# Kernel optimization log

Measured on AMD Instinct MI355X. Metric: run time of the kernel, lower is better.

The kernel has to match this reference:

```python
import jax, jax.numpy as jnp
import numpy as np

FP8_MAX = 448.0  # max finite value of float8_e4m3fn


def _fp8_quant(v, scale):
    # emulate saturating scaled cast to float8_e4m3fn, then dequant-free fp8 storage (upcast to f32 for the gemm)
    q = jnp.clip(v / scale, -FP8_MAX, FP8_MAX)
    return q.astype(jnp.float8_e4m3fn).astype(jnp.float32)


def setup_inputs() -> dict:
    key = jax.random.key(0)
    k0, k1, k2, k3 = jax.random.split(key, 4)
    T, H, I, E = 1024, 1024, 2816, 8
    x = jax.random.normal(k0, (T, H), jnp.float32)
    router_logits = jax.random.normal(k1, (T, E), jnp.float32)
    w13_weight = jax.random.normal(k2, (E, 2 * I, H), jnp.float32) * 0.02
    w2_weight = jax.random.normal(k3, (E, H, I), jnp.float32) * 0.02
    return {
        "x": x,
        "router_logits": router_logits,
        "w13_weight": w13_weight,
        "w2_weight": w2_weight,
        "w13_input_scale": jnp.ones((E,), jnp.float32),
        "w2_input_scale": jnp.ones((E,), jnp.float32),
        "top_k": 2,
    }


def reference(x, router_logits, w13_weight, w2_weight, w13_input_scale, w2_input_scale, top_k):
    T, H = x.shape
    E, two_I, _ = w13_weight.shape
    I = two_I // 2

    # --- routing: softmax -> top_k -> renormalize (select_experts) ---
    probs = jax.nn.softmax(router_logits, axis=-1)
    topk_w, topk_ids = jax.lax.top_k(probs, top_k)            # [T,K]
    topk_w = topk_w / jnp.sum(topk_w, axis=-1, keepdims=True)
    # dense combine matrix [T,E]: sparsity of the grouped gemm dispatch
    combine = jnp.zeros((T, E), x.dtype).at[jnp.arange(T)[:, None], topk_ids].add(topk_w)

    # --- per-expert fp8 weight quantization (ops.scaled_fp8_quant per expert) ---
    w13_scale = jnp.max(jnp.abs(w13_weight), axis=(1, 2)) / FP8_MAX  # [E]
    w2_scale = jnp.max(jnp.abs(w2_weight), axis=(1, 2)) / FP8_MAX
    w13_q = _fp8_quant(w13_weight, w13_scale[:, None, None])         # [E,2I,H]
    w2_q = _fp8_quant(w2_weight, w2_scale[:, None, None])            # [E,H,I]

    # --- grouped gemm 1: per-expert activation quant + fp8 gemm + dequant scale ---
    x_q = _fp8_quant(x[None], w13_input_scale[:, None, None])        # [E,T,H]
    h = jnp.einsum('eth,eih->eti', x_q, w13_q) * (w13_input_scale * w13_scale)[:, None, None]

    # --- silu_and_mul: gate = first intermediate_size rows, up = second ---
    act = jax.nn.silu(h[..., :I]) * h[..., I:]                       # [E,T,I]

    # --- grouped gemm 2 ---
    act_q = _fp8_quant(act, w2_input_scale[:, None, None])
    o = jnp.einsum('eti,ehi->eth', act_q, w2_q) * (w2_input_scale * w2_scale)[:, None, None]

    # --- post_reorder: weighted combine of selected experts ---
    return jnp.einsum('te,eth->th', combine, o)                      # [T,H]
```

## Files before the change

### kernel.cpp

```cpp
#include <hip/hip_runtime.h>
#include <cstdint>
#include <cstddef>

#define T_TOK 1024
#define H_DIM 1024
#define I_DIM 2816
#define E_NUM 8
#define PAIRS 2048
#define KSPLIT 4
#define NT1 (I_DIM / 16)
#define AMX2_X 32

typedef __attribute__((ext_vector_type(4))) float f32x4;
typedef __attribute__((ext_vector_type(4))) unsigned int u32x4;
typedef long i64;

__device__ __forceinline__ unsigned char fp8e4m3_sw(float v) {
  v = fminf(448.f, fmaxf(-448.f, v));
  unsigned b = __float_as_uint(v);
  unsigned s = (b >> 24) & 0x80u;
  float a = fabsf(v);
  if (a < 0.015625f) {
    int m = (int)rintf(a * 512.f);
    return (unsigned char)(s | (unsigned)m);
  }
  unsigned ab = b & 0x7fffffffu;
  unsigned rnd = 0x7FFFFu + ((ab >> 20) & 1u);
  ab += rnd;
  int e = (int)(ab >> 23) - 127;
  unsigned m = (ab >> 20) & 7u;
  if (e > 8 || (e == 8 && m > 6)) { e = 8; m = 6; }
  return (unsigned char)(s | (unsigned)((e + 7) << 3) | m);
}

__device__ __forceinline__ unsigned q4(float a, float b, float c, float d) {
#if __has_builtin(__builtin_amdgcn_cvt_pk_fp8_f32)
  unsigned w = (unsigned)__builtin_amdgcn_cvt_pk_fp8_f32(a, b, 0, false);
  return (unsigned)__builtin_amdgcn_cvt_pk_fp8_f32(c, d, (int)w, true);
#else
  return (unsigned)fp8e4m3_sw(a) | ((unsigned)fp8e4m3_sw(b) << 8) |
         ((unsigned)fp8e4m3_sw(c) << 16) | ((unsigned)fp8e4m3_sw(d) << 24);
#endif
}

__device__ __forceinline__ unsigned char q1(float a) {
#if __has_builtin(__builtin_amdgcn_cvt_pk_fp8_f32)
  return (unsigned char)((unsigned)__builtin_amdgcn_cvt_pk_fp8_f32(a, a, 0, false) & 0xFFu);
#else
  return fp8e4m3_sw(a);
#endif
}

__device__ __forceinline__ unsigned q4v(float4 f, float inv) {
  return q4(f.x * inv, f.y * inv, f.z * inv, f.w * inv);
}

__device__ __forceinline__ float wave_max(float m) {
#pragma unroll
  for (int off = 32; off > 0; off >>= 1) m = fmaxf(m, __shfl_xor(m, off));
  return m;
}

__global__ __launch_bounds__(256) void pre_k(const float* __restrict__ w13,
                                             const float* __restrict__ logits,
                                             float* __restrict__ part13,
                                             int* __restrict__ cnt_g,
                                             int* __restrict__ offs_g,
                                             int* __restrict__ pair_tok,
                                             float* __restrict__ pair_w,
                                             int* __restrict__ pairidx) {
  const int tid = threadIdx.x;
  if (blockIdx.x < 1024) {
    const int e = blockIdx.x >> 7, sub = blockIdx.x & 127;
    const float4* src = (const float4*)w13 + (size_t)e * (2 * I_DIM * H_DIM / 4);
    int idx = sub * 256 + tid;
    const int stride = 128 * 256;
    float m = 0.f;
#pragma unroll
    for (int j = 0; j < 44; j += 4) {
      float4 v0 = src[idx + (size_t)(j + 0) * stride];
      float4 v1 = src[idx + (size_t)(j + 1) * stride];
      float4 v2 = src[idx + (size_t)(j + 2) * stride];
      float4 v3 = src[idx + (size_t)(j + 3) * stride];
      m = fmaxf(m, fmaxf(fmaxf(fabsf(v0.x), fabsf(v0.y)), fmaxf(fabsf(v0.z), fabsf(v0.w))));
      m = fmaxf(m, fmaxf(fmaxf(fabsf(v1.x), fabsf(v1.y)), fmaxf(fabsf(v1.z), fabsf(v1.w))));
      m = fmaxf(m, fmaxf(fmaxf(fabsf(v2.x), fabsf(v2.y)), fmaxf(fabsf(v2.z), fabsf(v2.w))));
      m = fmaxf(m, fmaxf(fmaxf(fabsf(v3.x), fabsf(v3.y)), fmaxf(fabsf(v3.z), fabsf(v3.w))));
    }
    m = wave_max(m);
    __shared__ float wmax[4];
    int lane = tid & 63, wid = tid >> 6;
    if (lane == 0) wmax[wid] = m;
    __syncthreads();
    if (tid == 0)
      part13[blockIdx.x] = fmaxf(fmaxf(wmax[0], wmax[1]), fmaxf(wmax[2], wmax[3]));
    return;
  }

  __shared__ int cnt_s[E_NUM], pos_s[E_NUM];
  if (tid < E_NUM) cnt_s[tid] = 0;
  __syncthreads();
  int i0s[4], i1s[4];
  float w0s[4], w1s[4];
#pragma unroll
  for (int j = 0; j < 4; j++) {
    int t = tid * 4 + j;
    float l[E_NUM];
#pragma unroll
    for (int k = 0; k < E_NUM; k++) l[k] = logits[t * E_NUM + k];
    int i0 = 0; float b0 = l[0];
#pragma unroll
    for (int k = 1; k < E_NUM; k++) { if (l[k] > b0) { b0 = l[k]; i0 = k; } }
    int i1 = -1; float b1 = -3.4e38f;
#pragma unroll
    for (int k = 0; k < E_NUM; k++) { if (k != i0 && l[k] > b1) { b1 = l[k]; i1 = k; } }
    float e1 = expf(b1 - b0);
    float d = 1.f + e1;
    i0s[j] = i0; i1s[j] = i1; w0s[j] = 1.f / d; w1s[j] = e1 / d;
    atomicAdd(&cnt_s[i0], 1);
    atomicAdd(&cnt_s[i1], 1);
  }
  __syncthreads();
  if (tid == 0) {
    int s = 0;
#pragma unroll
    for (int e = 0; e < E_NUM; e++) {
      cnt_g[e] = cnt_s[e];
      offs_g[e] = s;
      pos_s[e] = s;
      s += cnt_s[e];
    }
    offs_g[E_NUM] = s;
  }
  __syncthreads();
#pragma unroll
  for (int j = 0; j < 4; j++) {
    int t = tid * 4 + j;
    int s0 = atomicAdd(&pos_s[i0s[j]], 1);
    pair_tok[s0] = t; pair_w[s0] = w0s[j]; pairidx[2 * t] = s0;
    int s1 = atomicAdd(&pos_s[i1s[j]], 1);
    pair_tok[s1] = t; pair_w[s1] = w1s[j]; pairidx[2 * t + 1] = s1;
  }
}

__global__ __launch_bounds__(256) void quantx_k(const float* __restrict__ x,
                                                const int* __restrict__ pair_tok,
                                                const int* __restrict__ offs,
                                                const float* __restrict__ s13,
                                                unsigned char* __restrict__ Xq) {
  int p = blockIdx.x;
  int t = pair_tok[p];
  int e = 0;
#pragma unroll
  for (int j = 1; j < E_NUM; j++) { if (p >= offs[j]) e = j; }
  float inv = 1.f / s13[e];
  float4 v = ((const float4*)(x + (size_t)t * H_DIM))[threadIdx.x];
  float a = fminf(448.f, fmaxf(-448.f, v.x * inv));
  float b = fminf(448.f, fmaxf(-448.f, v.y * inv));
  float c = fminf(448.f, fmaxf(-448.f, v.z * inv));
  float dd = fminf(448.f, fmaxf(-448.f, v.w * inv));
  ((unsigned*)(Xq + (size_t)p * H_DIM))[threadIdx.x] = q4(a, b, c, dd);
}

__global__ __launch_bounds__(512) void gemm1_k(const float* __restrict__ w13,
                                               const float* __restrict__ w2,
                                               const unsigned char* __restrict__ Xq,
                                               unsigned char* __restrict__ H1,
                                               const int* __restrict__ cnt,
                                               const int* __restrict__ offs,
                                               const float* __restrict__ part13,
                                               float* __restrict__ part2,
                                               const float* __restrict__ s13,
                                               const float* __restrict__ s2in) {
  const int e = blockIdx.z;
  const int tid = threadIdx.x, lane = tid & 63, wq = tid >> 6;

  if (blockIdx.x >= NT1) {
    const int bx2 = (blockIdx.x - NT1) * 4 + blockIdx.y;
    const float4* src = (const float4*)w2 + (size_t)e * (H_DIM * I_DIM / 4);
    int idx = bx2 * 512 + tid;
    const int stride = 128 * 512;
    float m = 0.f;
#pragma unroll
    for (int j = 0; j < 11; j++) {
      float4 v = src[idx + (size_t)j * stride];
      m = fmaxf(m, fmaxf(fmaxf(fabsf(v.x), fabsf(v.y)), fmaxf(fabsf(v.z), fabsf(v.w))));
    }
    m = wave_max(m);
    __shared__ float wmax2[8];
    if (lane == 0) wmax2[wq] = m;
    __syncthreads();
    if (tid == 0) {
      float mm = wmax2[0];
#pragma unroll
      for (int j = 1; j < 8; j++) mm = fmaxf(mm, wmax2[j]);
      part2[e * 128 + bx2] = mm;
    }
    return;
  }

  __shared__ float redA[8];
  {
    float v = part13[e * 128 + (tid & 127)];
    v = wave_max(v);
    if (lane == 0) redA[wq] = v;
  }
  __syncthreads();
  float amax = redA[0];
#pragma unroll
  for (int j = 1; j < 8; j++) amax = fmaxf(amax, redA[j]);

  const int count = cnt[e];
  const int m0 = blockIdx.y * 256;
  if (m0 >= count) return;
  const int nt = blockIdx.x;
  const int base = offs[e];

  const float inv_w = 448.f / amax;
  const float gs = s13[e] * (amax / 448.f);
  const float inv_a2 = 1.f / s2in[e];

  __shared__ __align__(16) unsigned char As[256][80];
  __shared__ __align__(16) unsigned char Bs[32][80];

  const int fr = lane & 15, ks = lane >> 4;

  f32x4 accg[2], accu[2];
#pragma unroll
  for (int i = 0; i < 2; i++) { accg[i] = (f32x4)0.f; accu[i] = (f32x4)0.f; }

  const int ar0 = tid >> 2, aseg = tid & 3;
  int pr0 = base + m0 + ar0;       if (pr0 > PAIRS - 1) pr0 = PAIRS - 1;
  int pr1 = base + m0 + ar0 + 128; if (pr1 > PAIRS - 1) pr1 = PAIRS - 1;
  const unsigned char* a_src0 = Xq + (size_t)pr0 * H_DIM + aseg * 16;
  const unsigned char* a_src1 = Xq + (size_t)pr1 * H_DIM + aseg * 16;

  const int brow = tid >> 4, bseg = tid & 15;
  const float* b_src = w13 + ((size_t)e * 2 * I_DIM + (size_t)nt * 16 +
                              (brow & 15) + (size_t)(brow >> 4) * I_DIM) * H_DIM + bseg * 4;

  u32x4 ra0 = *(const u32x4*)a_src0;
  u32x4 ra1 = *(const u32x4*)a_src1;
  float4 fb = ((const float4*)b_src)[0];
  unsigned qb = q4v(fb, inv_w);

  for (int t = 0; t < H_DIM / 64; ++t) {
    __syncthreads();
    *(u32x4*)&As[ar0][aseg * 16] = ra0;
    *(u32x4*)&As[ar0 + 128][aseg * 16] = ra1;
    *(unsigned*)&Bs[brow][bseg * 4] = qb;
    __syncthreads();
    if (t + 1 < H_DIM / 64) {
      int k0 = (t + 1) * 64;
      ra0 = *(const u32x4*)(a_src0 + k0);
      ra1 = *(const u32x4*)(a_src1 + k0);
      fb = *(const float4*)(b_src + k0);
    }
#pragma unroll
    for (int kk = 0; kk < 2; kk++) {
      i64 a0 = *(const i64*)&As[wq * 32 + fr][kk * 32 + ks * 8];
      i64 a1 = *(const i64*)&As[wq * 32 + 16 + fr][kk * 32 + ks * 8];
      i64 bg = *(const i64*)&Bs[fr][kk * 32 + ks * 8];
      i64 bu = *(const i64*)&Bs[16 + fr][kk * 32 + ks * 8];
      accg[0] = __builtin_amdgcn_mfma_f32_16x16x32_fp8_fp8(a0, bg, accg[0], 0, 0, 0);
      accg[1] = __builtin_amdgcn_mfma_f32_16x16x32_fp8_fp8(a1, bg, accg[1], 0, 0, 0);
      accu[0] = __builtin_amdgcn_mfma_f32_16x16x32_fp8_fp8(a0, bu, accu[0], 0, 0, 0);
      accu[1] = __builtin_amdgcn_mfma_f32_16x16x32_fp8_fp8(a1, bu, accu[1], 0, 0, 0);
    }
    qb = q4v(fb, inv_w);
  }

  const int rg = lane >> 4;
#pragma unroll
  for (int mi = 0; mi < 2; mi++) {
#pragma unroll
    for (int rr = 0; rr < 4; rr++) {
      int lrow = wq * 32 + mi * 16 + rg * 4 + rr;
      if (m0 + lrow < count) {
        size_t p = (size_t)(base + m0 + lrow);
        int col = nt * 16 + fr;
        float g = accg[mi][rr] * gs;
        float u = accu[mi][rr] * gs;
        float act = g / (1.f + expf(-g)) * u * inv_a2;
        act = fminf(448.f, fmaxf(-448.f, act));
        H1[p * I_DIM + col] = q1(act);
      }
    }
  }
}

__global__ __launch_bounds__(512) void gemm2_k(const float* __restrict__ w2,
                                               const unsigned char* __restrict__ H1,
                                               float* __restrict__ Op,
                                               const int* __restrict__ cnt,
                                               const int* __restrict__ offs,
                                               const float* __restrict__ part2,
                                               const float* __restrict__ s2in,
                                               const float* __restrict__ pair_w) {
  const int e = blockIdx.z;
  const int tid = threadIdx.x, lane = tid & 63, wq = tid >> 6;

  __shared__ float redA[8];
  {
    float v = part2[e * 128 + (tid & 127)];
    v = wave_max(v);
    if (lane == 0) redA[wq] = v;
  }
  __syncthreads();
  float amax = redA[0];
#pragma unroll
  for (int j = 1; j < 8; j++) amax = fmaxf(amax, redA[j]);

  const int count = cnt[e];
  const int m0 = blockIdx.y * 128;
  if (m0 >= count) return;
  const int nt = blockIdx.x & 15;
  const int ksp = blockIdx.x >> 4;
  const int n0 = nt * 64;
  const int base = offs[e];

  const float inv_w = 448.f / amax;
  const float s2 = s2in[e] * (amax / 448.f);

  __shared__ __align__(16) unsigned char As[2][128][80];
  __shared__ __align__(16) unsigned char Bs[2][64][80];

  const int fr = lane & 15, ks = lane >> 4;

  f32x4 acc[4];
#pragma unroll
  for (int i = 0; i < 4; i++) acc[i] = (f32x4)0.f;

  const int arow = tid >> 2, aseg = tid & 3;
  int pr = base + m0 + arow; if (pr > PAIRS - 1) pr = PAIRS - 1;
  const unsigned char* a_src = H1 + (size_t)pr * I_DIM + aseg * 16;

  const int brow = tid >> 3, bseg = tid & 7;
  const float* b_src = w2 + ((size_t)e * H_DIM + n0 + brow) * I_DIM + bseg * 8;

  const int KITER = (I_DIM / 64) / KSPLIT;
  const int kbase = ksp * KITER * 64;

  u32x4 ra = *(const u32x4*)(a_src + kbase);
  float4 fb0 = ((const float4*)(b_src + kbase))[0];
  float4 fb1 = ((const float4*)(b_src + kbase))[1];
  {
    unsigned qb0 = q4v(fb0, inv_w), qb1 = q4v(fb1, inv_w);
    *(u32x4*)&As[0][arow][aseg * 16] = ra;
    ((unsigned*)&Bs[0][brow][bseg * 8])[0] = qb0;
    ((unsigned*)&Bs[0][brow][bseg * 8])[1] = qb1;
  }
  {
    int k0 = kbase + 64;
    ra = *(const u32x4*)(a_src + k0);
    fb0 = ((const float4*)(b_src + k0))[0];
    fb1 = ((const float4*)(b_src + k0))[1];
  }
  __syncthreads();

  int c = 0;
  for (int t = 0; t < KITER; ++t) {
#pragma unroll
    for (int kk = 0; kk < 2; kk++) {
      i64 a0 = *(const i64*)&As[c][wq * 16 + fr][kk * 32 + ks * 8];
#pragma unroll
      for (int ni = 0; ni < 4; ni++) {
        i64 b = *(const i64*)&Bs[c][ni * 16 + fr][kk * 32 + ks * 8];
        acc[ni] = __builtin_amdgcn_mfma_f32_16x16x32_fp8_fp8(a0, b, acc[ni], 0, 0, 0);
      }
    }
    if (t + 1 < KITER) {
      unsigned qb0 = q4v(fb0, inv_w), qb1 = q4v(fb1, inv_w);
      *(u32x4*)&As[c ^ 1][arow][aseg * 16] = ra;
      ((unsigned*)&Bs[c ^ 1][brow][bseg * 8])[0] = qb0;
      ((unsigned*)&Bs[c ^ 1][brow][bseg * 8])[1] = qb1;
    }
    if (t + 2 < KITER) {
      int k0 = kbase + (t + 2) * 64;
      ra = *(const u32x4*)(a_src + k0);
      fb0 = ((const float4*)(b_src + k0))[0];
      fb1 = ((const float4*)(b_src + k0))[1];
    }
    __syncthreads();
    c ^= 1;
  }

  const int rg = lane >> 4;
#pragma unroll
  for (int rr = 0; rr < 4; rr++) {
    int lrow = wq * 16 + rg * 4 + rr;
    if (m0 + lrow < count) {
      size_t p = (size_t)(base + m0 + lrow);
      float pw = pair_w[p];
#pragma unroll
      for (int ni = 0; ni < 4; ni++) {
        int col = n0 + ni * 16 + fr;
        Op[((size_t)ksp * PAIRS + p) * H_DIM + col] = acc[ni][rr] * s2 * pw;
      }
    }
  }
}

__global__ __launch_bounds__(256) void combine_k(const float* __restrict__ Op,
                                                 const int* __restrict__ pairidx,
                                                 float* __restrict__ out) {
  int t = blockIdx.x;
  int p0 = pairidx[2 * t], p1 = pairidx[2 * t + 1];
  f32x4 acc = (f32x4)0.f;
#pragma unroll
  for (int s = 0; s < KSPLIT; s++) {
    f32x4 a = ((const f32x4*)(Op + ((size_t)s * PAIRS + p0) * H_DIM))[threadIdx.x];
    f32x4 b = ((const f32x4*)(Op + ((size_t)s * PAIRS + p1) * H_DIM))[threadIdx.x];
    acc += a + b;
  }
  ((f32x4*)(out + (size_t)t * H_DIM))[threadIdx.x] = acc;
}

extern "C" void kernel_launch(void* const* d_in, const int* in_sizes, int n_in,
                              void* d_out, int out_size, void* d_ws, size_t ws_size,
                              hipStream_t stream) {
  (void)in_sizes; (void)n_in; (void)out_size; (void)ws_size;
  const float* x      = (const float*)d_in[0];
  const float* logits = (const float*)d_in[1];
  const float* w13    = (const float*)d_in[2];
  const float* w2     = (const float*)d_in[3];
  const float* s13    = (const float*)d_in[4];
  const float* s2in   = (const float*)d_in[5];
  float* out = (float*)d_out;

  char* ws = (char*)d_ws;
  int* cnt      = (int*)(ws + 128);
  int* offs     = (int*)(ws + 192);
  float* part13 = (float*)(ws + 4096);
  float* part2  = (float*)(ws + 8192);
  int* pair_tok = (int*)(ws + 17408);
  float* pair_w = (float*)(ws + 25600);
  int* pairidx  = (int*)(ws + 33792);
  unsigned char* Xq = (unsigned char*)(ws + (size_t)(1 << 20));
  unsigned char* H1 = (unsigned char*)(ws + (size_t)4 * (1 << 20));
  float* Op         = (float*)(ws + (size_t)10 * (1 << 20));

  pre_k<<<1025, 256, 0, stream>>>(w13, logits, part13, cnt, offs,
                                  pair_tok, pair_w, pairidx);

  quantx_k<<<PAIRS, 256, 0, stream>>>(x, pair_tok, offs, s13, Xq);

  gemm1_k<<<dim3(NT1 + AMX2_X, 4, E_NUM), 512, 0, stream>>>(
      w13, w2, Xq, H1, cnt, offs, part13, part2, s13, s2in);

  gemm2_k<<<dim3(16 * KSPLIT, 8, E_NUM), 512, 0, stream>>>(
      w2, H1, Op, cnt, offs, part2, s2in, pair_w);

  combine_k<<<T_TOK, 256, 0, stream>>>(Op, pairidx, out);
}
```

Baseline: 173.7 us.

## Load A fragments directly to registers and widen gemm1 N tile to 32

Both grouped GEMM kernels stop staging the fp8 activation tile through shared memory. Each wave now loads its MFMA A fragments straight from global memory into registers and prefetches them one step ahead. Only the weight tile, which is quantized on the fly, still goes through LDS. Gemm1 also doubles its N tile from 16 to 32 columns per block (NT1 halved), which halves the number of times activations are re-read per expert. Gemm2 drops its LDS double buffer and goes back to a two-barrier single buffer. The direct global loads are 8-byte and less coalesced, and the single buffer may expose more latency.

```diff
diff --git a/kernel.cpp b/kernel.cpp
--- a/kernel.cpp
+++ b/kernel.cpp
@@ -8,7 +8,7 @@
 #define E_NUM 8
 #define PAIRS 2048
 #define KSPLIT 4
-#define NT1 (I_DIM / 16)
+#define NT1 (I_DIM / 32)
 #define AMX2_X 32
 
 typedef __attribute__((ext_vector_type(4))) float f32x4;
@@ -220,54 +220,60 @@
   const float gs = s13[e] * (amax / 448.f);
   const float inv_a2 = 1.f / s2in[e];
 
-  __shared__ __align__(16) unsigned char As[256][80];
-  __shared__ __align__(16) unsigned char Bs[32][80];
+  __shared__ __align__(16) unsigned char Bs[64][80];
 
   const int fr = lane & 15, ks = lane >> 4;
 
-  f32x4 accg[2], accu[2];
-#pragma unroll
-  for (int i = 0; i < 2; i++) { accg[i] = (f32x4)0.f; accu[i] = (f32x4)0.f; }
-
-  const int ar0 = tid >> 2, aseg = tid & 3;
-  int pr0 = base + m0 + ar0;       if (pr0 > PAIRS - 1) pr0 = PAIRS - 1;
-  int pr1 = base + m0 + ar0 + 128; if (pr1 > PAIRS - 1) pr1 = PAIRS - 1;
-  const unsigned char* a_src0 = Xq + (size_t)pr0 * H_DIM + aseg * 16;
-  const unsigned char* a_src1 = Xq + (size_t)pr1 * H_DIM + aseg * 16;
-
-  const int brow = tid >> 4, bseg = tid & 15;
-  const float* b_src = w13 + ((size_t)e * 2 * I_DIM + (size_t)nt * 16 +
-                              (brow & 15) + (size_t)(brow >> 4) * I_DIM) * H_DIM + bseg * 4;
-
-  u32x4 ra0 = *(const u32x4*)a_src0;
-  u32x4 ra1 = *(const u32x4*)a_src1;
-  float4 fb = ((const float4*)b_src)[0];
-  unsigned qb = q4v(fb, inv_w);
+  f32x4 accg[2][2], accu[2][2];
+#pragma unroll
+  for (int i = 0; i < 2; i++)
+#pragma unroll
+    for (int j = 0; j < 2; j++) { accg[i][j] = (f32x4)0.f; accu[i][j] = (f32x4)0.f; }
+
+  int rbse = base + m0 + wq * 32 + fr;
+  int r0 = rbse;      if (r0 > PAIRS - 1) r0 = PAIRS - 1;
+  int r1 = rbse + 16; if (r1 > PAIRS - 1) r1 = PAIRS - 1;
+  const unsigned char* a0p = Xq + (size_t)r0 * H_DIM + ks * 8;
+  const unsigned char* a1p = Xq + (size_t)r1 * H_DIM + ks * 8;
+
+  const int brow = tid >> 3, bseg = tid & 7;
+  const float* b_src = w13 + ((size_t)e * 2 * I_DIM + (size_t)nt * 32 +
+                              (brow & 31) + (size_t)(brow >> 5) * I_DIM) * H_DIM + bseg * 8;
+
+  float4 fb0 = ((const float4*)b_src)[0], fb1 = ((const float4*)b_src)[1];
+  unsigned qb0 = q4v(fb0, inv_w), qb1 = q4v(fb1, inv_w);
+  i64 a00 = *(const i64*)a0p,        a01 = *(const i64*)(a0p + 32);
+  i64 a10 = *(const i64*)a1p,        a11 = *(const i64*)(a1p + 32);
 
   for (int t = 0; t < H_DIM / 64; ++t) {
     __syncthreads();
-    *(u32x4*)&As[ar0][aseg * 16] = ra0;
-    *(u32x4*)&As[ar0 + 128][aseg * 16] = ra1;
-    *(unsigned*)&Bs[brow][bseg * 4] = qb;
-    __syncthreads();
+    ((unsigned*)&Bs[brow][bseg * 8])[0] = qb0;
+    ((unsigned*)&Bs[brow][bseg * 8])[1] = qb1;
+    __syncthreads();
+    i64 c00 = a00, c01 = a01, c10 = a10, c11 = a11;
     if (t + 1 < H_DIM / 64) {
       int k0 = (t + 1) * 64;
-      ra0 = *(const u32x4*)(a_src0 + k0);
-      ra1 = *(const u32x4*)(a_src1 + k0);
-      fb = *(const float4*)(b_src + k0);
+      fb0 = ((const float4*)(b_src + k0))[0];
+      fb1 = ((const float4*)(b_src + k0))[1];
+      a00 = *(const i64*)(a0p + k0); a01 = *(const i64*)(a0p + k0 + 32);
+      a10 = *(const i64*)(a1p + k0); a11 = *(const i64*)(a1p + k0 + 32);
     }
 #pragma unroll
     for (int kk = 0; kk < 2; kk++) {
-      i64 a0 = *(const i64*)&As[wq * 32 + fr][kk * 32 + ks * 8];
-      i64 a1 = *(const i64*)&As[wq * 32 + 16 + fr][kk * 32 + ks * 8];
-      i64 bg = *(const i64*)&Bs[fr][kk * 32 + ks * 8];
-      i64 bu = *(const i64*)&Bs[16 + fr][kk * 32 + ks * 8];
-      accg[0] = __builtin_amdgcn_mfma_f32_16x16x32_fp8_fp8(a0, bg, accg[0], 0, 0, 0);
-      accg[1] = __builtin_amdgcn_mfma_f32_16x16x32_fp8_fp8(a1, bg, accg[1], 0, 0, 0);
-      accu[0] = __builtin_amdgcn_mfma_f32_16x16x32_fp8_fp8(a0, bu, accu[0], 0, 0, 0);
-      accu[1] = __builtin_amdgcn_mfma_f32_16x16x32_fp8_fp8(a1, bu, accu[1], 0, 0, 0);
-    }
-    qb = q4v(fb, inv_w);
+      i64 af0 = kk ? c01 : c00;
+      i64 af1 = kk ? c11 : c10;
+#pragma unroll
+      for (int ni = 0; ni < 2; ni++) {
+        i64 bg = *(const i64*)&Bs[ni * 16 + fr][kk * 32 + ks * 8];
+        i64 bu = *(const i64*)&Bs[32 + ni * 16 + fr][kk * 32 + ks * 8];
+        accg[0][ni] = __builtin_amdgcn_mfma_f32_16x16x32_fp8_fp8(af0, bg, accg[0][ni], 0, 0, 0);
+        accg[1][ni] = __builtin_amdgcn_mfma_f32_16x16x32_fp8_fp8(af1, bg, accg[1][ni], 0, 0, 0);
+        accu[0][ni] = __builtin_amdgcn_mfma_f32_16x16x32_fp8_fp8(af0, bu, accu[0][ni], 0, 0, 0);
+        accu[1][ni] = __builtin_amdgcn_mfma_f32_16x16x32_fp8_fp8(af1, bu, accu[1][ni], 0, 0, 0);
+      }
+    }
+    qb0 = q4v(fb0, inv_w);
+    qb1 = q4v(fb1, inv_w);
   }
 
   const int rg = lane >> 4;
@@ -278,12 +284,15 @@
       int lrow = wq * 32 + mi * 16 + rg * 4 + rr;
       if (m0 + lrow < count) {
         size_t p = (size_t)(base + m0 + lrow);
-        int col = nt * 16 + fr;
-        float g = accg[mi][rr] * gs;
-        float u = accu[mi][rr] * gs;
-        float act = g / (1.f + expf(-g)) * u * inv_a2;
-        act = fminf(448.f, fmaxf(-448.f, act));
-        H1[p * I_DIM + col] = q1(act);
+#pragma unroll
+        for (int ni = 0; ni < 2; ni++) {
+          int col = nt * 32 + ni * 16 + fr;
+          float g = accg[mi][ni][rr] * gs;
+          float u = accu[mi][ni][rr] * gs;
+          float act = g / (1.f + expf(-g)) * u * inv_a2;
+          act = fminf(448.f, fmaxf(-448.f, act));
+          H1[p * I_DIM + col] = q1(act);
+        }
       }
     }
   }
@@ -322,67 +331,51 @@
   const float inv_w = 448.f / amax;
   const float s2 = s2in[e] * (amax / 448.f);
 
-  __shared__ __align__(16) unsigned char As[2][128][80];
-  __shared__ __align__(16) unsigned char Bs[2][64][80];
+  __shared__ __align__(16) unsigned char Bs[64][80];
 
   const int fr = lane & 15, ks = lane >> 4;
 
   f32x4 acc[4];
 #pragma unroll
   for (int i = 0; i < 4; i++) acc[i] = (f32x4)0.f;
-
-  const int arow = tid >> 2, aseg = tid & 3;
-  int pr = base + m0 + arow; if (pr > PAIRS - 1) pr = PAIRS - 1;
-  const unsigned char* a_src = H1 + (size_t)pr * I_DIM + aseg * 16;
-
-  const int brow = tid >> 3, bseg = tid & 7;
-  const float* b_src = w2 + ((size_t)e * H_DIM + n0 + brow) * I_DIM + bseg * 8;
 
   const int KITER = (I_DIM / 64) / KSPLIT;
   const int kbase = ksp * KITER * 64;
 
-  u32x4 ra = *(const u32x4*)(a_src + kbase);
-  float4 fb0 = ((const float4*)(b_src + kbase))[0];
-  float4 fb1 = ((const float4*)(b_src + kbase))[1];
-  {
-    unsigned qb0 = q4v(fb0, inv_w), qb1 = q4v(fb1, inv_w);
-    *(u32x4*)&As[0][arow][aseg * 16] = ra;
-    ((unsigned*)&Bs[0][brow][bseg * 8])[0] = qb0;
-    ((unsigned*)&Bs[0][brow][bseg * 8])[1] = qb1;
-  }
-  {
-    int k0 = kbase + 64;
-    ra = *(const u32x4*)(a_src + k0);
-    fb0 = ((const float4*)(b_src + k0))[0];
-    fb1 = ((const float4*)(b_src + k0))[1];
-  }
-  __syncthreads();
-
-  int c = 0;
+  int rbse = base + m0 + wq * 16 + fr;
+  int r0 = rbse; if (r0 > PAIRS - 1) r0 = PAIRS - 1;
+  const unsigned char* ap = H1 + (size_t)r0 * I_DIM + kbase + ks * 8;
+
+  const int brow = tid >> 3, bseg = tid & 7;
+  const float* b_src = w2 + ((size_t)e * H_DIM + n0 + brow) * I_DIM + kbase + bseg * 8;
+
+  float4 fb0 = ((const float4*)b_src)[0], fb1 = ((const float4*)b_src)[1];
+  unsigned qb0 = q4v(fb0, inv_w), qb1 = q4v(fb1, inv_w);
+  i64 a0 = *(const i64*)ap, a1 = *(const i64*)(ap + 32);
+
   for (int t = 0; t < KITER; ++t) {
-#pragma unroll
-    for (int kk = 0; kk < 2; kk++) {
-      i64 a0 = *(const i64*)&As[c][wq * 16 + fr][kk * 32 + ks * 8];
-#pragma unroll
-      for (int ni = 0; ni < 4; ni++) {
-        i64 b = *(const i64*)&Bs[c][ni * 16 + fr][kk * 32 + ks * 8];
-        acc[ni] = __builtin_amdgcn_mfma_f32_16x16x32_fp8_fp8(a0, b, acc[ni], 0, 0, 0);
-      }
-    }
+    __syncthreads();
+    ((unsigned*)&Bs[brow][bseg * 8])[0] = qb0;
+    ((unsigned*)&Bs[brow][bseg * 8])[1] = qb1;
+    __syncthreads();
+    i64 c0 = a0, c1 = a1;
     if (t + 1 < KITER) {
-      unsigned qb0 = q4v(fb0, inv_w), qb1 = q4v(fb1, inv_w);
-      *(u32x4*)&As[c ^ 1][arow][aseg * 16] = ra;
-      ((unsigned*)&Bs[c ^ 1][brow][bseg * 8])[0] = qb0;
-      ((unsigned*)&Bs[c ^ 1][brow][bseg * 8])[1] = qb1;
-    }
-    if (t + 2 < KITER) {
-      int k0 = kbase + (t + 2) * 64;
-      ra = *(const u32x4*)(a_src + k0);
+      int k0 = (t + 1) * 64;
       fb0 = ((const float4*)(b_src + k0))[0];
       fb1 = ((const float4*)(b_src + k0))[1];
-    }
-    __syncthreads();
-    c ^= 1;
+      a0 = *(const i64*)(ap + k0); a1 = *(const i64*)(ap + k0 + 32);
+    }
+#pragma unroll
+    for (int kk = 0; kk < 2; kk++) {
+      i64 af = kk ? c1 : c0;
+#pragma unroll
+      for (int ni = 0; ni < 4; ni++) {
+        i64 b = *(const i64*)&Bs[ni * 16 + fr][kk * 32 + ks * 8];
+        acc[ni] = __builtin_amdgcn_mfma_f32_16x16x32_fp8_fp8(af, b, acc[ni], 0, 0, 0);
+      }
+    }
+    qb0 = q4v(fb0, inv_w);
+    qb1 = q4v(fb1, inv_w);
   }
 
   const int rg = lane >> 4;
```

After: 202.8 us. +16.7%, slower.
